# Optimization experiments

Hardware: AMD Instinct MI355X
Metric: run time of the kernel (lower is better)

Reference implementation:

```python
import jax, jax.numpy as jnp
import numpy as np

B, H, L, D, S = 4, 16, 4096, 64, 128

def setup_inputs() -> dict:
    key = jax.random.key(0)
    k1, k2 = jax.random.split(key)
    x = jax.random.normal(k1, (B, H, L, D), dtype=jnp.float32)
    c = jax.random.normal(k2, (H, S, D), dtype=jnp.float32)
    # codebook rows are unit-normalized at init (matches torch init)
    c = c / jnp.linalg.norm(c, axis=-1, keepdims=True)
    return {"x": x, "c": c}

def reference(x, c):
    # cosine-similarity scores: [B,H,L,S]
    cos_sim = jnp.einsum('bhld,hsd->bhls', x, c)
    delta_index = jnp.argmax(cos_sim, axis=-1)            # [B,H,L]
    delta_onehot = jax.nn.one_hot(delta_index, c.shape[-2], dtype=jnp.float32)  # [B,H,L,S]
    return (delta_onehot, c)
```

## Files before the change

### kernel.cpp

```cpp
#include <hip/hip_runtime.h>
#include <math.h>

constexpr int BB = 4;
constexpr int HH = 16;
constexpr int LL = 4096;
constexpr int DD = 64;
constexpr int SS = 128;
constexpr int BM = 128;
constexpr int GG = 2;

constexpr float TAU = 2e-3f;

typedef __attribute__((ext_vector_type(8))) short bf16x8;
typedef __attribute__((ext_vector_type(4))) float f32x4;

#define MFMA16 __builtin_amdgcn_mfma_f32_16x16x32_bf16

__device__ __forceinline__ unsigned short f2bf(float v) {
    unsigned u = __float_as_uint(v);
    return (unsigned short)((u + 0x7fffu + ((u >> 16) & 1u)) >> 16);
}

__device__ __forceinline__ void split8(const float4 va, const float4 vb,
                                       uint4* hi, uint4* lo) {
    const float v[8] = {va.x, va.y, va.z, va.w, vb.x, vb.y, vb.z, vb.w};
    unsigned hw[4], lw[4];
    #pragma unroll
    for (int p = 0; p < 4; ++p) {
        const unsigned u0 = __float_as_uint(v[2 * p]);
        const unsigned u1 = __float_as_uint(v[2 * p + 1]);
        const unsigned h0 = u0 & 0xffff0000u;
        const unsigned h1 = u1 & 0xffff0000u;
        hw[p] = (u0 >> 16) | h1;
        lw[p] = (unsigned)f2bf(v[2 * p] - __uint_as_float(h0))
              | ((unsigned)f2bf(v[2 * p + 1] - __uint_as_float(h1)) << 16);
    }
    *hi = make_uint4(hw[0], hw[1], hw[2], hw[3]);
    *lo = make_uint4(lw[0], lw[1], lw[2], lw[3]);
}

union FragU { uint4 q; bf16x8 v; };

__global__ __launch_bounds__(256) void convert_c_kernel(
    const float* __restrict__ c, unsigned char* __restrict__ ws,
    float* __restrict__ out_c)
{
    const int sid = blockIdx.x * 256 + threadIdx.x;
    const int h  = sid >> 10;
    const int r  = sid & 1023;
    const int kt = r >> 9;
    const int ct = (r >> 6) & 7;
    const int ln = r & 63;
    const int cc = ct * 16 + (ln & 15);
    const int k0 = kt * 32 + (ln >> 4) * 8;
    const float4* src = (const float4*)(c + ((size_t)h * SS + cc) * DD + k0);
    uint4 hi, lo;
    split8(src[0], src[1], &hi, &lo);
    unsigned char* base =
        ws + (size_t)h * 32768 + (size_t)(((kt << 3) | ct) * 1024 + ln * 16);
    *(uint4*)(base) = hi;
    *(uint4*)(base + 16384) = lo;

    const f32x4* __restrict__ s4 = (const f32x4*)c;
    f32x4* __restrict__ d4 = (f32x4*)out_c;
    __builtin_nontemporal_store(s4[sid], d4 + sid);
    __builtin_nontemporal_store(s4[sid + 16384], d4 + sid + 16384);
}

__device__ __forceinline__ void load_a(const float* __restrict__ x,
                                       long long rbase, int wv, int lane,
                                       float4* raw) {
    const int ln15 = lane & 15;
    const int k0 = (lane >> 4) * 8;
    #pragma unroll
    for (int rtb = 0; rtb < 2; ++rtb) {
        const float* xr =
            x + (size_t)(rbase + wv * 32 + rtb * 16 + ln15) * DD + k0;
        #pragma unroll
        for (int kt = 0; kt < 2; ++kt) {
            raw[rtb * 4 + kt * 2 + 0] = *(const float4*)(xr + kt * 32);
            raw[rtb * 4 + kt * 2 + 1] = *(const float4*)(xr + kt * 32 + 4);
        }
    }
}

__device__ __forceinline__ void split_a(const float4* raw, bf16x8 af[2][2][2]) {
    #pragma unroll
    for (int rtb = 0; rtb < 2; ++rtb)
        #pragma unroll
        for (int kt = 0; kt < 2; ++kt) {
            FragU hi, lo;
            split8(raw[rtb * 4 + kt * 2], raw[rtb * 4 + kt * 2 + 1],
                   &hi.q, &lo.q);
            af[rtb][kt][0] = hi.v;
            af[rtb][kt][1] = lo.v;
        }
}

template <bool USE_WS>
__global__ __launch_bounds__(256, 2) void quantizer_kernel(
    const float* __restrict__ x,
    const float* __restrict__ c,
    const unsigned char* __restrict__ ws,
    float* __restrict__ out,
    float* __restrict__ out_c)
{
    __shared__ __align__(16) unsigned char smemB[32768];
    __shared__ int amax[BM];
    __shared__ int s_nflag;
    __shared__ int s_flag[BM];
    __shared__ float s_fsc[SS];

    const int tid = threadIdx.x;
    const int wv = tid >> 6;
    const int lane = tid & 63;
    const int ln15 = lane & 15;
    const int blk = blockIdx.x;
    const long long base0 = (long long)blk * (GG * BM);
    const int h = (int)((base0 >> 12) & (HH - 1));
    const float* __restrict__ chead = c + (size_t)h * SS * DD;

    if (tid == 0) s_nflag = 0;

    if (USE_WS) {
        const unsigned char* wsb = ws + (size_t)h * 32768;
        #pragma unroll
        for (int it = 0; it < 8; ++it) {
            const unsigned off = (unsigned)(wv * 8192 + it * 1024);
            __builtin_amdgcn_global_load_lds(
                (const __attribute__((address_space(1))) unsigned*)
                    (wsb + off + (unsigned)(lane * 16)),
                (__attribute__((address_space(3))) unsigned*)(smemB + off),
                16, 0, 0);
        }
    } else {
        #pragma unroll
        for (int it = 0; it < 4; ++it) {
            const int sid = it * 256 + tid;
            const int kt = sid >> 9;
            const int ct = (sid >> 6) & 7;
            const int ln = sid & 63;
            const int cc = ct * 16 + (ln & 15);
            const int k0 = kt * 32 + (ln >> 4) * 8;
            const float4* src = (const float4*)(chead + (size_t)cc * DD + k0);
            uint4 hi, lo;
            split8(src[0], src[1], &hi, &lo);
            unsigned char* dst = smemB + ((kt << 3) | ct) * 1024 + ln * 16;
            *(uint4*)dst = hi;
            *(uint4*)(dst + 16384) = lo;
        }
    }

    float4 xraw[8];
    load_a(x, base0, wv, lane, xraw);
    bf16x8 af[2][2][2];
    split_a(xraw, af);

    __syncthreads();

    #pragma unroll
    for (int g = 0; g < GG; ++g) {
        const long long rg = base0 + (long long)g * BM;

        if (g + 1 < GG) load_a(x, base0 + (long long)(g + 1) * BM,
                               wv, lane, xraw);

        float m1[2][4], m2[2][4];
        int   mi_[2][4];
        #pragma unroll
        for (int rtb = 0; rtb < 2; ++rtb)
            #pragma unroll
            for (int r = 0; r < 4; ++r) {
                m1[rtb][r] = -INFINITY; m2[rtb][r] = -INFINITY;
                mi_[rtb][r] = 0;
            }

        #pragma unroll
        for (int ct = 0; ct < 8; ++ct) {
            const unsigned bb = (unsigned)(ct << 10) + (unsigned)(lane * 16);
            const bf16x8 b10 = *(const bf16x8*)(smemB + bb);
            const bf16x8 b11 = *(const bf16x8*)(smemB + bb + 8192);
            const bf16x8 b20 = *(const bf16x8*)(smemB + bb + 16384);
            const bf16x8 b21 = *(const bf16x8*)(smemB + bb + 24576);
            #pragma unroll
            for (int rtb = 0; rtb < 2; ++rtb) {
                f32x4 a0 = {0.f, 0.f, 0.f, 0.f};
                f32x4 a1 = {0.f, 0.f, 0.f, 0.f};
                a0 = MFMA16(af[rtb][0][1], b10, a0, 0, 0, 0);
                a0 = MFMA16(af[rtb][0][0], b20, a0, 0, 0, 0);
                a0 = MFMA16(af[rtb][0][0], b10, a0, 0, 0, 0);
                a1 = MFMA16(af[rtb][1][1], b11, a1, 0, 0, 0);
                a1 = MFMA16(af[rtb][1][0], b21, a1, 0, 0, 0);
                a1 = MFMA16(af[rtb][1][0], b11, a1, 0, 0, 0);
                #pragma unroll
                for (int r = 0; r < 4; ++r) {
                    const float v = a0[r] + a1[r];
                    const int col = ct * 16 + ln15;
                    m2[rtb][r] =
                        __builtin_amdgcn_fmed3f(m1[rtb][r], v, m2[rtb][r]);
                    if (v > m1[rtb][r]) { m1[rtb][r] = v; mi_[rtb][r] = col; }
                }
            }
        }

        #pragma unroll
        for (int rtb = 0; rtb < 2; ++rtb) {
            #pragma unroll
            for (int r = 0; r < 4; ++r) {
                float a1 = m1[rtb][r], a2 = m2[rtb][r];
                int ai = mi_[rtb][r];
                #pragma unroll
                for (int off = 1; off <= 8; off <<= 1) {
                    const float o1 = __shfl_xor(a1, off);
                    const float o2 = __shfl_xor(a2, off);
                    const int   oi = __shfl_xor(ai, off);
                    const bool take = (o1 > a1) || (o1 == a1 && oi < ai);
                    const float n2 = take ? fmaxf(a1, o2) : fmaxf(a2, o1);
                    if (take) { a1 = o1; ai = oi; }
                    a2 = n2;
                }
                if (ln15 == 0) {
                    const int row = (2 * wv + rtb) * 16 + (lane >> 4) * 4 + r;
                    if (a1 - a2 >= TAU) {
                        amax[row] = ai;
                    } else {
                        const int p = atomicAdd(&s_nflag, 1);
                        s_flag[p] = row;
                    }
                }
            }
        }
        __syncthreads();

        const int nf = s_nflag;
        for (int f = 0; f < nf; ++f) {
            const int row = s_flag[f];
            if (tid < SS) {
                const float4* __restrict__ xr =
                    (const float4*)(x + (size_t)(rg + row) * DD);
                const float4* __restrict__ cr =
                    (const float4*)(chead + (size_t)tid * DD);
                float sc = 0.f;
                #pragma unroll
                for (int q = 0; q < 16; ++q) {
                    const float4 a = xr[q];
                    const float4 b = cr[q];
                    sc = fmaf(a.x, b.x, sc); sc = fmaf(a.y, b.y, sc);
                    sc = fmaf(a.z, b.z, sc); sc = fmaf(a.w, b.w, sc);
                }
                s_fsc[tid] = sc;
            }
            __syncthreads();
            if (tid == 0) {
                float bv = s_fsc[0]; int bi = 0;
                for (int s = 1; s < SS; ++s)
                    if (s_fsc[s] > bv) { bv = s_fsc[s]; bi = s; }
                amax[row] = bi;
            }
            __syncthreads();
        }
        if (tid == 0) s_nflag = 0;

        f32x4* __restrict__ op = (f32x4*)(out + (size_t)rg * SS);
        #pragma unroll 4
        for (int i = tid; i < BM * (SS / 4); i += 256) {
            const int rr = i >> 5;
            const int s0 = (i & 31) * 4;
            const int am = amax[rr];
            f32x4 v = {(s0 + 0 == am) ? 1.f : 0.f,
                       (s0 + 1 == am) ? 1.f : 0.f,
                       (s0 + 2 == am) ? 1.f : 0.f,
                       (s0 + 3 == am) ? 1.f : 0.f};
            __builtin_nontemporal_store(v, op + i);
        }
        __syncthreads();

        if (g + 1 < GG) split_a(xraw, af);
    }

    if (!USE_WS && blk < 128) {
        const float4* __restrict__ src = (const float4*)c;
        float4* __restrict__ dst = (float4*)out_c;
        const int idx = blk * 256 + tid;
        dst[idx] = src[idx];
    }
}

extern "C" void kernel_launch(void* const* d_in, const int* in_sizes, int n_in,
                              void* d_out, int out_size, void* d_ws, size_t ws_size,
                              hipStream_t stream) {
    const float* x = (const float*)d_in[0];
    const float* c = (const float*)d_in[1];
    float* out = (float*)d_out;
    float* out_c = out + (size_t)BB * HH * LL * SS;

    const int rows = BB * HH * LL;
    const int blocks = rows / (GG * BM);
    const size_t ws_need = (size_t)HH * 32768;

    if (d_ws != nullptr && ws_size >= ws_need) {
        convert_c_kernel<<<64, 256, 0, stream>>>(c, (unsigned char*)d_ws,
                                                 out_c);
        quantizer_kernel<true><<<blocks, 256, 0, stream>>>(
            x, c, (const unsigned char*)d_ws, out, out_c);
    } else {
        quantizer_kernel<false><<<blocks, 256, 0, stream>>>(
            x, c, nullptr, out, out_c);
    }
}
```

Before: 212.6 us.

## Resolve ambiguous argmax rows per wavefront and double-buffer amax

The fallback for rows whose bf16 top-two margin is below tolerance moves from a block-wide loop to per-wavefront lists. Each wave now recomputes its own flagged rows in fp32, with 64 lanes covering 128 codes and a shuffle argmax. This drops the two __syncthreads per flagged row and the serial single-thread scan. amax is indexed by group, which lets the trailing barrier after the store loop be removed. The cost is a wave-local count reset that depends on in-wave ordering and on one barrier per group.

```diff
diff --git a/kernel.cpp b/kernel.cpp
--- a/kernel.cpp
+++ b/kernel.cpp
@@ -106,10 +106,9 @@
     float* __restrict__ out_c)
 {
     __shared__ __align__(16) unsigned char smemB[32768];
-    __shared__ int amax[BM];
-    __shared__ int s_nflag;
-    __shared__ int s_flag[BM];
-    __shared__ float s_fsc[SS];
+    __shared__ int amax[GG][BM];
+    __shared__ int s_wcnt[4];
+    __shared__ int s_wlist[4][32];
 
     const int tid = threadIdx.x;
     const int wv = tid >> 6;
@@ -119,8 +118,6 @@
     const long long base0 = (long long)blk * (GG * BM);
     const int h = (int)((base0 >> 12) & (HH - 1));
     const float* __restrict__ chead = c + (size_t)h * SS * DD;
-
-    if (tid == 0) s_nflag = 0;
 
     if (USE_WS) {
         const unsigned char* wsb = ws + (size_t)h * 32768;
@@ -161,6 +158,9 @@
     #pragma unroll
     for (int g = 0; g < GG; ++g) {
         const long long rg = base0 + (long long)g * BM;
+        int* __restrict__ amaxg = amax[g];
+
+        if (lane == 0) s_wcnt[wv] = 0;
 
         if (g + 1 < GG) load_a(x, base0 + (long long)(g + 1) * BM,
                                wv, lane, xraw);
@@ -222,58 +222,59 @@
                 if (ln15 == 0) {
                     const int row = (2 * wv + rtb) * 16 + (lane >> 4) * 4 + r;
                     if (a1 - a2 >= TAU) {
-                        amax[row] = ai;
+                        amaxg[row] = ai;
                     } else {
-                        const int p = atomicAdd(&s_nflag, 1);
-                        s_flag[p] = row;
+                        const int p = atomicAdd(&s_wcnt[wv], 1);
+                        s_wlist[wv][p] = row;
                     }
                 }
             }
         }
+
+        const int cnt = s_wcnt[wv];
+        for (int f = 0; f < cnt; ++f) {
+            const int row = s_wlist[wv][f];
+            const float4* __restrict__ xr =
+                (const float4*)(x + (size_t)(rg + row) * DD);
+            const float4* __restrict__ c0 =
+                (const float4*)(chead + (size_t)lane * DD);
+            const float4* __restrict__ c1 =
+                (const float4*)(chead + (size_t)(lane + 64) * DD);
+            float s0 = 0.f, s1 = 0.f;
+            #pragma unroll
+            for (int q = 0; q < 16; ++q) {
+                const float4 a = xr[q];
+                const float4 b0 = c0[q];
+                const float4 b1 = c1[q];
+                s0 = fmaf(a.x, b0.x, s0); s0 = fmaf(a.y, b0.y, s0);
+                s0 = fmaf(a.z, b0.z, s0); s0 = fmaf(a.w, b0.w, s0);
+                s1 = fmaf(a.x, b1.x, s1); s1 = fmaf(a.y, b1.y, s1);
+                s1 = fmaf(a.z, b1.z, s1); s1 = fmaf(a.w, b1.w, s1);
+            }
+            float v = s0; int bi = lane;
+            if (s1 > v) { v = s1; bi = lane + 64; }
+            #pragma unroll
+            for (int off = 1; off < 64; off <<= 1) {
+                const float ov = __shfl_xor(v, off);
+                const int   oi = __shfl_xor(bi, off);
+                if (ov > v || (ov == v && oi < bi)) { v = ov; bi = oi; }
+            }
+            if (lane == 0) amaxg[row] = bi;
+        }
         __syncthreads();
-
-        const int nf = s_nflag;
-        for (int f = 0; f < nf; ++f) {
-            const int row = s_flag[f];
-            if (tid < SS) {
-                const float4* __restrict__ xr =
-                    (const float4*)(x + (size_t)(rg + row) * DD);
-                const float4* __restrict__ cr =
-                    (const float4*)(chead + (size_t)tid * DD);
-                float sc = 0.f;
-                #pragma unroll
-                for (int q = 0; q < 16; ++q) {
-                    const float4 a = xr[q];
-                    const float4 b = cr[q];
-                    sc = fmaf(a.x, b.x, sc); sc = fmaf(a.y, b.y, sc);
-                    sc = fmaf(a.z, b.z, sc); sc = fmaf(a.w, b.w, sc);
-                }
-                s_fsc[tid] = sc;
-            }
-            __syncthreads();
-            if (tid == 0) {
-                float bv = s_fsc[0]; int bi = 0;
-                for (int s = 1; s < SS; ++s)
-                    if (s_fsc[s] > bv) { bv = s_fsc[s]; bi = s; }
-                amax[row] = bi;
-            }
-            __syncthreads();
-        }
-        if (tid == 0) s_nflag = 0;
 
         f32x4* __restrict__ op = (f32x4*)(out + (size_t)rg * SS);
         #pragma unroll 4
         for (int i = tid; i < BM * (SS / 4); i += 256) {
             const int rr = i >> 5;
             const int s0 = (i & 31) * 4;
-            const int am = amax[rr];
+            const int am = amaxg[rr];
             f32x4 v = {(s0 + 0 == am) ? 1.f : 0.f,
                        (s0 + 1 == am) ? 1.f : 0.f,
                        (s0 + 2 == am) ? 1.f : 0.f,
                        (s0 + 3 == am) ? 1.f : 0.f};
             __builtin_nontemporal_store(v, op + i);
         }
-        __syncthreads();
 
         if (g + 1 < GG) split_a(xraw, af);
     }
```

Result: faster. 202.1 us (-4.9%).
